# Performance work log

Measured on AMD Instinct MI355X. Metric: run time of the kernel, lower is better.

The kernel has to match this reference:

```python
import jax, jax.numpy as jnp
import numpy as np

V = 50257   # vocab_size
BLOCK = 1024
D = 768     # n_embd
H = 12      # n_head
L = 2       # n_layer
B = 4
T = 1024
EPS = 1e-5


def _ln(x, g, b):
    mu = jnp.mean(x, axis=-1, keepdims=True)
    var = jnp.var(x, axis=-1, keepdims=True)
    return (x - mu) * jax.lax.rsqrt(var + EPS) * g + b


def setup_inputs() -> dict:
    key = jax.random.key(0)
    ks = jax.random.split(key, 10)
    def n(k, shape, std=0.02):
        return jax.random.normal(k, shape, jnp.float32) * std
    proj_std = (2 * L) ** -0.5  # set_scale init in the torch code
    return dict(
        idx=jax.random.randint(ks[0], (B, T), 0, V),
        layer_num=0,
        wte=n(ks[1], (V, D)),
        wpe=n(ks[2], (BLOCK, D)),
        ln1_g=jnp.ones((L, D)), ln1_b=jnp.zeros((L, D)),
        attn_w=n(ks[3], (L, D, 3 * D)), attn_b=jnp.zeros((L, 3 * D)),
        proj_w=n(ks[4], (L, D, D), proj_std), proj_b=jnp.zeros((L, D)),
        ln2_g=jnp.ones((L, D)), ln2_b=jnp.zeros((L, D)),
        fc_w=n(ks[5], (L, D, 4 * D)), fc_b=jnp.zeros((L, 4 * D)),
        fc2_w=n(ks[6], (L, 4 * D, D), proj_std), fc2_b=jnp.zeros((L, D)),
        lnf_g=jnp.ones((D,)), lnf_b=jnp.zeros((D,)),
        lm_w=n(ks[7], (D, V)),
    )


def _gpt(idx, wte, wpe, ln1_g, ln1_b, attn_w, attn_b, proj_w, proj_b,
         ln2_g, ln2_b, fc_w, fc_b, fc2_w, fc2_b, lnf_g, lnf_b, lm_w):
    b, t = idx.shape
    hd = D // H
    x = wte[idx] + wpe[:t]                      # [B,T,D]
    causal = jnp.tril(jnp.ones((t, t), bool))   # [T,T]
    for l in range(L):
        h = _ln(x, ln1_g[l], ln1_b[l])
        qkv = h @ attn_w[l] + attn_b[l]          # [B,T,3D]
        q, k, v = jnp.split(qkv, 3, axis=-1)
        q = q.reshape(b, t, H, hd)
        k = k.reshape(b, t, H, hd)
        v = v.reshape(b, t, H, hd)
        att = jnp.einsum('bqhd,bkhd->bhqk', q, k) * (1.0 / np.sqrt(hd))
        att = jnp.where(causal, att, -jnp.inf)
        att = jax.nn.softmax(att, axis=-1)
        y = jnp.einsum('bhqk,bkhd->bqhd', att, v).reshape(b, t, D)
        x = x + (y @ proj_w[l] + proj_b[l])
        h2 = _ln(x, ln2_g[l], ln2_b[l])
        h2 = jax.nn.gelu(h2 @ fc_w[l] + fc_b[l], approximate=True)  # tanh GELU
        x = x + (h2 @ fc2_w[l] + fc2_b[l])
    x = _ln(x, lnf_g, lnf_b)
    return x @ lm_w                             # [B,T,V] logits


def reference(idx, layer_num, wte, wpe, ln1_g, ln1_b, attn_w, attn_b,
              proj_w, proj_b, ln2_g, ln2_b, fc_w, fc_b, fc2_w, fc2_b,
              lnf_g, lnf_b, lm_w):
    # layer_num is unused in the forward math (pipeline-stage bookkeeping)
    return _gpt(idx, wte, wpe, ln1_g, ln1_b, attn_w, attn_b, proj_w, proj_b,
                ln2_g, ln2_b, fc_w, fc_b, fc2_w, fc2_b, lnf_g, lnf_b, lm_w)
```

## Files before the change

kernel.cpp:

```cpp
#include <hip/hip_runtime.h>
#include <hip/hip_bf16.h>
#include <cstdint>
#include <cstddef>

typedef __bf16 bf16_t;
typedef __bf16 bf16x8 __attribute__((ext_vector_type(8)));
typedef float f32x4 __attribute__((ext_vector_type(4)));

#define GLB_AS(p) ((__attribute__((address_space(1))) void*)(void*)(p))
#define LDS_AS(p) ((__attribute__((address_space(3))) void*)(p))
#define PIN(x) asm volatile("" : "+v"(x))

__device__ __forceinline__ float wave_red_sum(float v) {
#pragma unroll
  for (int o = 1; o < 64; o <<= 1) v += __shfl_xor(v, o, 64);
  return v;
}

__device__ __forceinline__ float gelu_tanh(float v) {
  float c = 0.7978845608028654f * (v + 0.044715f * v * v * v);
  return 0.5f * v * (1.0f + tanhf(c));
}

__device__ __forceinline__ f32x4 mfma16(f32x4 a, f32x4 b, f32x4 c) {
  return __builtin_amdgcn_mfma_f32_16x16x32_bf16(
      __builtin_bit_cast(bf16x8, a), __builtin_bit_cast(bf16x8, b), c, 0, 0, 0);
}

__device__ __forceinline__ int swz(int off) { return off ^ ((off >> 3) & 0x70); }

__global__ __launch_bounds__(256) void embed_k(const int* __restrict__ idx,
                                               const float* __restrict__ wte,
                                               const float* __restrict__ wpe,
                                               float* __restrict__ x) {
  const int m = blockIdx.x;
  const int tid = threadIdx.x;
  const int tok = idx[m];
  const int t = m & 1023;
#pragma unroll
  for (int i = 0; i < 3; ++i) {
    const int d = tid + i * 256;
    x[(size_t)m * 768 + d] = wte[(size_t)tok * 768 + d] + wpe[(size_t)t * 768 + d];
  }
}

__global__ __launch_bounds__(256) void ln_k(const float* __restrict__ x,
                                            const float* __restrict__ g,
                                            const float* __restrict__ b,
                                            bf16_t* __restrict__ out) {
  const int row = blockIdx.x;
  const int tid = threadIdx.x;
  const float* xr = x + (size_t)row * 768;
  float v0 = xr[tid], v1 = xr[tid + 256], v2 = xr[tid + 512];
  float s = v0 + v1 + v2;
  float q = v0 * v0 + v1 * v1 + v2 * v2;
  s = wave_red_sum(s);
  q = wave_red_sum(q);
  __shared__ float sm[8];
  const int wave = tid >> 6, lane = tid & 63;
  if (lane == 0) { sm[wave] = s; sm[4 + wave] = q; }
  __syncthreads();
  s = sm[0] + sm[1] + sm[2] + sm[3];
  q = sm[4] + sm[5] + sm[6] + sm[7];
  const float mu = s * (1.0f / 768.0f);
  const float var = q * (1.0f / 768.0f) - mu * mu;
  const float rs = rsqrtf(var + 1e-5f);
  bf16_t* orow = out + (size_t)row * 768;
#pragma unroll
  for (int i = 0; i < 3; ++i) {
    const int d = tid + i * 256;
    const float v = (i == 0 ? v0 : (i == 1 ? v1 : v2));
    orow[d] = (bf16_t)((v - mu) * rs * g[d] + b[d]);
  }
}

__global__ __launch_bounds__(256) void transp_k(const float* __restrict__ W,
                                                bf16_t* __restrict__ WT,
                                                int K, int N, int Npad) {
  __shared__ float tile[32][33];
  const int n0 = blockIdx.x * 32, k0 = blockIdx.y * 32;
  const int tx = threadIdx.x, ty = threadIdx.y;
#pragma unroll
  for (int i = 0; i < 4; ++i) {
    const int k = k0 + ty + i * 8, n = n0 + tx;
    tile[ty + i * 8][tx] = (k < K && n < N) ? W[(size_t)k * N + n] : 0.0f;
  }
  __syncthreads();
#pragma unroll
  for (int i = 0; i < 4; ++i) {
    const int n = n0 + ty + i * 8, k = k0 + tx;
    if (n < Npad && k < K) WT[(size_t)n * K + k] = (bf16_t)tile[tx][ty + i * 8];
  }
}

__global__ __launch_bounds__(256) void vtr_k(const bf16_t* __restrict__ qkv,
                                             bf16_t* __restrict__ vt) {
  __shared__ bf16_t tile[64][72];
  const int bh = blockIdx.y;
  const int h = bh % 12, b = bh / 12;
  const int t0 = blockIdx.x * 64;
  const int tx = threadIdx.x & 63;
  const int wv = threadIdx.x >> 6;
#pragma unroll
  for (int i = 0; i < 16; ++i) {
    const int r = wv * 16 + i;
    tile[r][tx] = qkv[(size_t)(b * 1024 + t0 + r) * 2304 + 1536 + h * 64 + tx];
  }
  __syncthreads();
#pragma unroll
  for (int i = 0; i < 16; ++i) {
    const int d = wv * 16 + i;
    vt[((size_t)bh * 64 + d) * 1024 + t0 + tx] = tile[tx][d];
  }
}

template <int EPI>
__global__ __launch_bounds__(512, 2) void gemm256(const bf16_t* __restrict__ A,
                                                  const bf16_t* __restrict__ BT,
                                                  const float* __restrict__ bias,
                                                  void* __restrict__ outp,
                                                  int M, int N, int K, int Nout) {
  __shared__ __align__(16) char lds[131072];
  const int tid = threadIdx.x;
  const int lane = tid & 63, wave = tid >> 6;
  const int wr = wave >> 2, wc = wave & 3;
  const int fr = lane & 15, fq = lane >> 4;

  const int nmblk = M >> 8;
  const int nwg = gridDim.x;
  const int flat = blockIdx.x;
  const int xcd = flat & 7, rest = flat >> 3;
  const int q8 = nwg >> 3, r8 = nwg & 7;
  const int wgid = (xcd < r8 ? xcd * (q8 + 1) : r8 * (q8 + 1) + (xcd - r8) * q8) + rest;
  const int m0 = (wgid % nmblk) << 8;
  const int n0 = (wgid / nmblk) << 8;

  const int NT = K >> 6;

  int srow[4], scb[4];
#pragma unroll
  for (int u = 0; u < 4; ++u) {
    const int s = swz(u * 8192 + tid * 16);
    srow[u] = s >> 7;
    scb[u] = s & 127;
  }
  const char* Abase = (const char*)A;
  const char* Bbase = (const char*)BT;

  auto stageA = [&](int pi, int u, int tau) {
    const char* src = Abase + ((size_t)(m0 + srow[u]) * K + tau * 64) * 2 + scb[u];
    __builtin_amdgcn_global_load_lds(GLB_AS(src),
        LDS_AS(&lds[pi * 32768 + u * 8192 + wave * 1024]), 16, 0, 0);
  };
  auto stageB = [&](int pi, int u, int tau) {
    const char* src = Bbase + ((size_t)(n0 + srow[u]) * K + tau * 64) * 2 + scb[u];
    __builtin_amdgcn_global_load_lds(GLB_AS(src),
        LDS_AS(&lds[65536 + pi * 32768 + u * 8192 + wave * 1024]), 16, 0, 0);
  };
  auto rdA = [&](int pi, int msub, int i, int kk) -> f32x4 {
    const int row = wr * 128 + msub * 64 + i * 16 + fr;
    const int off = swz(row * 128 + kk * 64 + fq * 16);
    return *(const f32x4*)(&lds[pi * 32768 + off]);
  };
  auto rdB = [&](int pi, int j, int kk) -> f32x4 {
    const int row = wc * 64 + j * 16 + fr;
    const int off = swz(row * 128 + kk * 64 + fq * 16);
    return *(const f32x4*)(&lds[65536 + pi * 32768 + off]);
  };

  f32x4 acc[8][4] = {};
  f32x4 a_[4][2], b_[4][2];

  stageA(0, 0, 0); stageA(0, 1, 0); stageA(0, 2, 0); stageA(0, 3, 0);
  stageB(0, 0, 0); stageB(0, 1, 0); stageB(0, 2, 0); stageB(0, 3, 0);
  stageA(1, 0, 1); stageA(1, 2, 1); stageB(1, 0, 1); stageB(1, 1, 1);
  stageA(1, 1, 1); stageA(1, 3, 1);
  asm volatile("s_waitcnt vmcnt(6)" ::: "memory");
  __builtin_amdgcn_s_barrier();

  int pi = 0;
  for (int tau = 0; tau < NT; ++tau) {
#pragma unroll
    for (int i = 0; i < 4; ++i) { a_[i][0] = rdA(pi, 0, i, 0); a_[i][1] = rdA(pi, 0, i, 1); }
#pragma unroll
    for (int j = 0; j < 4; ++j) { b_[j][0] = rdB(pi, j, 0); b_[j][1] = rdB(pi, j, 1); }
#pragma unroll
    for (int i = 0; i < 4; ++i) { PIN(a_[i][0]); PIN(a_[i][1]); }
#pragma unroll
    for (int j = 0; j < 4; ++j) { PIN(b_[j][0]); PIN(b_[j][1]); }
    if (tau + 1 < NT) { stageB(pi ^ 1, 2, tau + 1); stageB(pi ^ 1, 3, tau + 1); }
    __builtin_amdgcn_s_barrier();
    __builtin_amdgcn_s_setprio(1);
#pragma unroll
    for (int i = 0; i < 4; ++i)
#pragma unroll
      for (int j = 0; j < 2; ++j) {
        acc[i][j] = mfma16(a_[i][0], b_[j][0], acc[i][j]);
        acc[i][j] = mfma16(a_[i][1], b_[j][1], acc[i][j]);
      }
    __builtin_amdgcn_s_setprio(0);
    __builtin_amdgcn_s_barrier();
    if (tau + 2 < NT) { stageA(pi, 0, tau + 2); stageA(pi, 2, tau + 2); }
    __builtin_amdgcn_s_barrier();
    __builtin_amdgcn_s_setprio(1);
#pragma unroll
    for (int i = 0; i < 4; ++i)
#pragma unroll
      for (int j = 0; j < 2; ++j) {
        acc[i][2 + j] = mfma16(a_[i][0], b_[2 + j][0], acc[i][2 + j]);
        acc[i][2 + j] = mfma16(a_[i][1], b_[2 + j][1], acc[i][2 + j]);
      }
    __builtin_amdgcn_s_setprio(0);
    __builtin_amdgcn_s_barrier();
#pragma unroll
    for (int i = 0; i < 4; ++i) { a_[i][0] = rdA(pi, 1, i, 0); a_[i][1] = rdA(pi, 1, i, 1); }
#pragma unroll
    for (int i = 0; i < 4; ++i) { PIN(a_[i][0]); PIN(a_[i][1]); }
    if (tau + 2 < NT) { stageB(pi, 0, tau + 2); stageB(pi, 1, tau + 2); }
    __builtin_amdgcn_s_barrier();
    __builtin_amdgcn_s_setprio(1);
#pragma unroll
    for (int i = 0; i < 4; ++i)
#pragma unroll
      for (int j = 0; j < 2; ++j) {
        acc[4 + i][j] = mfma16(a_[i][0], b_[j][0], acc[4 + i][j]);
        acc[4 + i][j] = mfma16(a_[i][1], b_[j][1], acc[4 + i][j]);
      }
    __builtin_amdgcn_s_setprio(0);
    __builtin_amdgcn_s_barrier();
    if (tau + 2 < NT) {
      stageA(pi, 1, tau + 2); stageA(pi, 3, tau + 2);
      asm volatile("s_waitcnt vmcnt(6)" ::: "memory");
    } else {
      asm volatile("s_waitcnt vmcnt(0)" ::: "memory");
    }
    __builtin_amdgcn_s_barrier();
    __builtin_amdgcn_s_setprio(1);
#pragma unroll
    for (int i = 0; i < 4; ++i)
#pragma unroll
      for (int j = 0; j < 2; ++j) {
        acc[4 + i][2 + j] = mfma16(a_[i][0], b_[2 + j][0], acc[4 + i][2 + j]);
        acc[4 + i][2 + j] = mfma16(a_[i][1], b_[2 + j][1], acc[4 + i][2 + j]);
      }
    __builtin_amdgcn_s_setprio(0);
    __builtin_amdgcn_s_barrier();
    pi ^= 1;
  }

#pragma unroll
  for (int i8 = 0; i8 < 8; ++i8) {
#pragma unroll
    for (int j4 = 0; j4 < 4; ++j4) {
      const int r0 = m0 + wr * 128 + i8 * 16 + fq * 4;
      const int c = n0 + wc * 64 + j4 * 16 + fr;
      float bv = 0.0f;
      if constexpr (EPI != 3) bv = bias[c];
#pragma unroll
      for (int e = 0; e < 4; ++e) {
        const int r = r0 + e;
        float v = acc[i8][j4][e] + bv;
        if constexpr (EPI == 0) {
          ((bf16_t*)outp)[(size_t)r * N + c] = (bf16_t)v;
        } else if constexpr (EPI == 1) {
          ((bf16_t*)outp)[(size_t)r * N + c] = (bf16_t)gelu_tanh(v);
        } else {
          if (c < Nout) ((float*)outp)[(size_t)r * Nout + c] = v;
        }
      }
    }
  }
}

template <int EPI>
__global__ __launch_bounds__(256) void gemm_bt(const bf16_t* __restrict__ A,
                                               const bf16_t* __restrict__ BT,
                                               const float* __restrict__ bias,
                                               void* __restrict__ outp,
                                               float* __restrict__ resid,
                                               int M, int N, int K, int Nout) {
  __shared__ __align__(16) bf16_t As[128 * 32];
  __shared__ __align__(16) bf16_t Bs[128 * 32];
  const int tid = threadIdx.x;
  const int lane = tid & 63, wave = tid >> 6;

  const int nmblk = M >> 7;
  const int nwg = gridDim.x;
  const int flat = blockIdx.x;
  const int xcd = flat & 7, rest = flat >> 3;
  const int q8 = nwg >> 3, r8 = nwg & 7;
  const int wgid = (xcd < r8 ? xcd * (q8 + 1) : r8 * (q8 + 1) + (xcd - r8) * q8) + rest;
  const int m0 = (wgid % nmblk) * 128;
  const int n0 = (wgid / nmblk) * 128;

  const int wr = wave >> 1, wc = wave & 1;
  const int fr = lane & 15, fq = lane >> 4;
  const int se = tid * 8;
  const int srow = se >> 5, scol = se & 31;
  const int wvbase = wave * 512;
  f32x4 acc[4][4] = {};

  for (int k0 = 0; k0 < K; k0 += 32) {
#pragma unroll
    for (int r = 0; r < 2; ++r) {
      __builtin_amdgcn_global_load_lds(
          GLB_AS(&A[(size_t)(m0 + srow + r * 64) * K + k0 + scol]),
          LDS_AS(&As[wvbase + r * 2048]), 16, 0, 0);
      __builtin_amdgcn_global_load_lds(
          GLB_AS(&BT[(size_t)(n0 + srow + r * 64) * K + k0 + scol]),
          LDS_AS(&Bs[wvbase + r * 2048]), 16, 0, 0);
    }
    __syncthreads();
    bf16x8 a[4], b[4];
#pragma unroll
    for (int i = 0; i < 4; ++i) {
      a[i] = *(const bf16x8*)(&As[(wr * 64 + i * 16 + fr) * 32 + fq * 8]);
      b[i] = *(const bf16x8*)(&Bs[(wc * 64 + i * 16 + fr) * 32 + fq * 8]);
    }
#pragma unroll
    for (int i = 0; i < 4; ++i)
#pragma unroll
      for (int j = 0; j < 4; ++j)
        acc[i][j] = __builtin_amdgcn_mfma_f32_16x16x32_bf16(a[i], b[j], acc[i][j], 0, 0, 0);
    __syncthreads();
  }

#pragma unroll
  for (int i = 0; i < 4; ++i) {
#pragma unroll
    for (int j = 0; j < 4; ++j) {
      const int r0 = m0 + wr * 64 + i * 16 + fq * 4;
      const int c = n0 + wc * 64 + j * 16 + fr;
      const float bv = bias[c];
#pragma unroll
      for (int e = 0; e < 4; ++e) {
        const int r = r0 + e;
        resid[(size_t)r * N + c] += acc[i][j][e] + bv;
      }
    }
  }
}

__global__ __launch_bounds__(256) void fattn_k(const bf16_t* __restrict__ qkv,
                                               const bf16_t* __restrict__ vt,
                                               bf16_t* __restrict__ y) {
  __shared__ bf16_t Pl[4][16][40];
  const int wave = threadIdx.x >> 6, lane = threadIdx.x & 63;
  const int wid = blockIdx.x * 4 + wave;
  const int qt = wid & 63;
  const int bh = wid >> 6;
  const int h = bh % 12, b = bh / 12;
  const int fr = lane & 15, fq = lane >> 4;

  const bf16_t* qrow = qkv + (size_t)(b * 1024 + qt * 16 + fr) * 2304 + h * 64;
  const bf16x8 qf0 = *(const bf16x8*)(qrow + fq * 8);
  const bf16x8 qf1 = *(const bf16x8*)(qrow + 32 + fq * 8);

  const bf16_t* kbase = qkv + (size_t)b * 1024 * 2304 + 768 + h * 64 + fq * 8;
  const bf16_t* vbase = vt + ((size_t)bh * 64 + fr) * 1024 + fq * 8;

  f32x4 o[4] = {};
  float mrun[4], lrun[4];
#pragma unroll
  for (int e = 0; e < 4; ++e) { mrun[e] = -1e30f; lrun[e] = 0.0f; }

  const int qg = qt * 16 + fq * 4;
  const int kv_end = qt * 16 + 16;

  for (int kv0 = 0; kv0 < kv_end; kv0 += 32) {
    f32x4 s0 = {}, s1 = {};
    {
      const bf16_t* k0p = kbase + (size_t)(kv0 + fr) * 2304;
      const bf16_t* k1p = kbase + (size_t)(kv0 + 16 + fr) * 2304;
      const bf16x8 kf00 = *(const bf16x8*)(k0p);
      const bf16x8 kf01 = *(const bf16x8*)(k0p + 32);
      const bf16x8 kf10 = *(const bf16x8*)(k1p);
      const bf16x8 kf11 = *(const bf16x8*)(k1p + 32);
      s0 = __builtin_amdgcn_mfma_f32_16x16x32_bf16(qf0, kf00, s0, 0, 0, 0);
      s0 = __builtin_amdgcn_mfma_f32_16x16x32_bf16(qf1, kf01, s0, 0, 0, 0);
      s1 = __builtin_amdgcn_mfma_f32_16x16x32_bf16(qf0, kf10, s1, 0, 0, 0);
      s1 = __builtin_amdgcn_mfma_f32_16x16x32_bf16(qf1, kf11, s1, 0, 0, 0);
    }
    float v0[4], v1[4];
#pragma unroll
    for (int e = 0; e < 4; ++e) {
      v0[e] = (kv0 + fr <= qg + e) ? s0[e] * 0.125f : -1e30f;
      v1[e] = (kv0 + 16 + fr <= qg + e) ? s1[e] * 0.125f : -1e30f;
    }
    float p0[4], p1[4];
#pragma unroll
    for (int e = 0; e < 4; ++e) {
      float mx = fmaxf(v0[e], v1[e]);
      mx = fmaxf(mx, __shfl_xor(mx, 1, 64));
      mx = fmaxf(mx, __shfl_xor(mx, 2, 64));
      mx = fmaxf(mx, __shfl_xor(mx, 4, 64));
      mx = fmaxf(mx, __shfl_xor(mx, 8, 64));
      const float mnew = fmaxf(mrun[e], mx);
      p0[e] = __expf(v0[e] - mnew);
      p1[e] = __expf(v1[e] - mnew);
      float rs = p0[e] + p1[e];
      rs += __shfl_xor(rs, 1, 64);
      rs += __shfl_xor(rs, 2, 64);
      rs += __shfl_xor(rs, 4, 64);
      rs += __shfl_xor(rs, 8, 64);
      const float alpha = __expf(mrun[e] - mnew);
      lrun[e] = lrun[e] * alpha + rs;
      mrun[e] = mnew;
#pragma unroll
      for (int db = 0; db < 4; ++db) o[db][e] *= alpha;
    }
#pragma unroll
    for (int e = 0; e < 4; ++e) {
      Pl[wave][fq * 4 + e][fr] = (bf16_t)p0[e];
      Pl[wave][fq * 4 + e][16 + fr] = (bf16_t)p1[e];
    }
    asm volatile("s_waitcnt lgkmcnt(0)" ::: "memory");
    const bf16x8 pf = *(const bf16x8*)(&Pl[wave][fr][fq * 8]);
#pragma unroll
    for (int db = 0; db < 4; ++db) {
      const bf16x8 vf = *(const bf16x8*)(vbase + (size_t)db * 16 * 1024 + kv0);
      o[db] = __builtin_amdgcn_mfma_f32_16x16x32_bf16(pf, vf, o[db], 0, 0, 0);
    }
  }

#pragma unroll
  for (int db = 0; db < 4; ++db) {
#pragma unroll
    for (int e = 0; e < 4; ++e) {
      const int q = qt * 16 + fq * 4 + e;
      const int d = db * 16 + fr;
      y[(size_t)(b * 1024 + q) * 768 + h * 64 + d] = (bf16_t)(o[db][e] / lrun[e]);
    }
  }
}

extern "C" void kernel_launch(void* const* d_in, const int* in_sizes, int n_in,
                              void* d_out, int out_size, void* d_ws, size_t ws_size,
                              hipStream_t stream) {
  constexpr int Bb = 4, T = 1024, Lg = 2, Vr = 50257, Vp = 50432;
  constexpr int M = Bb * T;

  const int* idx = (const int*)d_in[0];
  const float* wte = (const float*)d_in[2];
  const float* wpe = (const float*)d_in[3];
  const float* ln1_g = (const float*)d_in[4];
  const float* ln1_b = (const float*)d_in[5];
  const float* attn_w = (const float*)d_in[6];
  const float* attn_b = (const float*)d_in[7];
  const float* proj_w = (const float*)d_in[8];
  const float* proj_b = (const float*)d_in[9];
  const float* ln2_g = (const float*)d_in[10];
  const float* ln2_b = (const float*)d_in[11];
  const float* fc_w = (const float*)d_in[12];
  const float* fc_b = (const float*)d_in[13];
  const float* fc2_w = (const float*)d_in[14];
  const float* fc2_b = (const float*)d_in[15];
  const float* lnf_g = (const float*)d_in[16];
  const float* lnf_b = (const float*)d_in[17];
  const float* lm_w = (const float*)d_in[18];
  float* out = (float*)d_out;

  char* wp = (char*)d_ws;
  auto take = [&](size_t n) { char* p = wp; wp += (n + 255) & ~(size_t)255; return p; };
  bf16_t* WqkvT = (bf16_t*)take((size_t)Lg * 2304 * 768 * 2);
  bf16_t* WprojT = (bf16_t*)take((size_t)Lg * 768 * 768 * 2);
  bf16_t* WfcT = (bf16_t*)take((size_t)Lg * 3072 * 768 * 2);
  bf16_t* Wfc2T = (bf16_t*)take((size_t)Lg * 768 * 3072 * 2);
  bf16_t* WlmT = (bf16_t*)take((size_t)Vp * 768 * 2);
  float* xb = (float*)take((size_t)M * 768 * 4);
  bf16_t* hb = (bf16_t*)take((size_t)M * 768 * 2);
  bf16_t* qkvb = (bf16_t*)take((size_t)M * 2304 * 2);
  bf16_t* yb = (bf16_t*)take((size_t)M * 768 * 2);
  bf16_t* actb = (bf16_t*)take((size_t)M * 3072 * 2);
  bf16_t* vtb = (bf16_t*)take((size_t)M * 768 * 2);

  const dim3 tb(32, 8);
  for (int l = 0; l < Lg; ++l) {
    transp_k<<<dim3(2304 / 32, 768 / 32), tb, 0, stream>>>(
        attn_w + (size_t)l * 768 * 2304, WqkvT + (size_t)l * 2304 * 768, 768, 2304, 2304);
    transp_k<<<dim3(768 / 32, 768 / 32), tb, 0, stream>>>(
        proj_w + (size_t)l * 768 * 768, WprojT + (size_t)l * 768 * 768, 768, 768, 768);
    transp_k<<<dim3(3072 / 32, 768 / 32), tb, 0, stream>>>(
        fc_w + (size_t)l * 768 * 3072, WfcT + (size_t)l * 3072 * 768, 768, 3072, 3072);
    transp_k<<<dim3(768 / 32, 3072 / 32), tb, 0, stream>>>(
        fc2_w + (size_t)l * 3072 * 768, Wfc2T + (size_t)l * 768 * 3072, 3072, 768, 768);
  }
  transp_k<<<dim3(Vp / 32, 768 / 32), tb, 0, stream>>>(lm_w, WlmT, 768, Vr, Vp);

  embed_k<<<M, 256, 0, stream>>>(idx, wte, wpe, xb);

  for (int l = 0; l < Lg; ++l) {
    ln_k<<<M, 256, 0, stream>>>(xb, ln1_g + l * 768, ln1_b + l * 768, hb);
    gemm256<0><<<(M / 256) * (2304 / 256), 512, 0, stream>>>(
        hb, WqkvT + (size_t)l * 2304 * 768, attn_b + l * 2304, qkvb, M, 2304, 768, 2304);
    vtr_k<<<dim3(T / 64, Bb * 12), 256, 0, stream>>>(qkvb, vtb);
    fattn_k<<<(Bb * 12 * 64) / 4, 256, 0, stream>>>(qkvb, vtb, yb);
    gemm_bt<2><<<(M / 128) * (768 / 128), 256, 0, stream>>>(
        yb, WprojT + (size_t)l * 768 * 768, proj_b + l * 768, nullptr, xb,
        M, 768, 768, 768);
    ln_k<<<M, 256, 0, stream>>>(xb, ln2_g + l * 768, ln2_b + l * 768, hb);
    gemm256<1><<<(M / 256) * (3072 / 256), 512, 0, stream>>>(
        hb, WfcT + (size_t)l * 3072 * 768, fc_b + l * 3072, actb, M, 3072, 768, 3072);
    gemm_bt<2><<<(M / 128) * (768 / 128), 256, 0, stream>>>(
        actb, Wfc2T + (size_t)l * 768 * 3072, fc2_b + l * 768, nullptr, xb,
        M, 768, 3072, 768);
  }
  ln_k<<<M, 256, 0, stream>>>(xb, lnf_g, lnf_b, hb);
  gemm256<3><<<(M / 256) * (Vp / 256), 512, 0, stream>>>(
      hb, WlmT, nullptr, out, M, Vp, 768, Vr);
}
```

Before: 1.249 ms.

## Make 256-tile GEMM persistent with cross-tile prefetch pipelining

Converts the 256x256 GEMM into a persistent kernel where each workgroup processes a contiguous range of output tiles. The global-to-LDS prefetch keeps running across tile boundaries, so the loads for the next tile overlap the current tile's tail and epilogue. The LM head now launches a fixed grid of 512 workgroups instead of one per tile, which cuts launch waves and tail effects. The QKV and FC GEMMs keep one tile per block. The cost is extra index bookkeeping per k-step and a serialized epilogue inside each workgroup.

```diff
diff --git a/kernel.cpp b/kernel.cpp
--- a/kernel.cpp
+++ b/kernel.cpp
@@ -115,11 +115,12 @@
 }
 
 template <int EPI>
-__global__ __launch_bounds__(512, 2) void gemm256(const bf16_t* __restrict__ A,
-                                                  const bf16_t* __restrict__ BT,
-                                                  const float* __restrict__ bias,
-                                                  void* __restrict__ outp,
-                                                  int M, int N, int K, int Nout) {
+__global__ __launch_bounds__(512, 2) void gemm256p(const bf16_t* __restrict__ A,
+                                                   const bf16_t* __restrict__ BT,
+                                                   const float* __restrict__ bias,
+                                                   void* __restrict__ outp,
+                                                   int M, int N, int K, int Nout,
+                                                   int ntiles) {
   __shared__ __align__(16) char lds[131072];
   const int tid = threadIdx.x;
   const int lane = tid & 63, wave = tid >> 6;
@@ -127,15 +128,17 @@
   const int fr = lane & 15, fq = lane >> 4;
 
   const int nmblk = M >> 8;
-  const int nwg = gridDim.x;
+  const int G = gridDim.x;
   const int flat = blockIdx.x;
   const int xcd = flat & 7, rest = flat >> 3;
-  const int q8 = nwg >> 3, r8 = nwg & 7;
-  const int wgid = (xcd < r8 ? xcd * (q8 + 1) : r8 * (q8 + 1) + (xcd - r8) * q8) + rest;
-  const int m0 = (wgid % nmblk) << 8;
-  const int n0 = (wgid / nmblk) << 8;
-
+  const int q8 = G >> 3, r8 = G & 7;
+  const int bid = (xcd < r8 ? xcd * (q8 + 1) : r8 * (q8 + 1) + (xcd - r8) * q8) + rest;
+  const int qt = ntiles / G, rt = ntiles % G;
+  const int tstart = bid * qt + (bid < rt ? bid : rt);
+  const int cnt = qt + (bid < rt ? 1 : 0);
+  if (cnt == 0) return;
   const int NT = K >> 6;
+  const int sEnd = (tstart + cnt) * NT;
 
   int srow[4], scb[4];
 #pragma unroll
@@ -147,13 +150,13 @@
   const char* Abase = (const char*)A;
   const char* Bbase = (const char*)BT;
 
-  auto stageA = [&](int pi, int u, int tau) {
-    const char* src = Abase + ((size_t)(m0 + srow[u]) * K + tau * 64) * 2 + scb[u];
+  auto stageA = [&](int pi, int u, int m0x, int tauK) {
+    const char* src = Abase + ((size_t)(m0x + srow[u]) * K + tauK * 64) * 2 + scb[u];
     __builtin_amdgcn_global_load_lds(GLB_AS(src),
         LDS_AS(&lds[pi * 32768 + u * 8192 + wave * 1024]), 16, 0, 0);
   };
-  auto stageB = [&](int pi, int u, int tau) {
-    const char* src = Bbase + ((size_t)(n0 + srow[u]) * K + tau * 64) * 2 + scb[u];
+  auto stageB = [&](int pi, int u, int n0x, int tauK) {
+    const char* src = Bbase + ((size_t)(n0x + srow[u]) * K + tauK * 64) * 2 + scb[u];
     __builtin_amdgcn_global_load_lds(GLB_AS(src),
         LDS_AS(&lds[65536 + pi * 32768 + u * 8192 + wave * 1024]), 16, 0, 0);
   };
@@ -168,107 +171,125 @@
     return *(const f32x4*)(&lds[65536 + pi * 32768 + off]);
   };
 
+  int m0 = (tstart % nmblk) << 8, n0 = (tstart / nmblk) << 8;
+  int m1 = m0, n1 = n0, t1 = 1;
+  int m2 = m0, n2 = n0, t2 = 2;
+  auto adv = [&](int& mx, int& nx, int& tx) {
+    if (++tx == NT) { tx = 0; mx += 256; if (mx >= M) { mx = 0; nx += 256; } }
+  };
+
   f32x4 acc[8][4] = {};
   f32x4 a_[4][2], b_[4][2];
 
-  stageA(0, 0, 0); stageA(0, 1, 0); stageA(0, 2, 0); stageA(0, 3, 0);
-  stageB(0, 0, 0); stageB(0, 1, 0); stageB(0, 2, 0); stageB(0, 3, 0);
-  stageA(1, 0, 1); stageA(1, 2, 1); stageB(1, 0, 1); stageB(1, 1, 1);
-  stageA(1, 1, 1); stageA(1, 3, 1);
+  stageA(0, 0, m0, 0); stageA(0, 1, m0, 0); stageA(0, 2, m0, 0); stageA(0, 3, m0, 0);
+  stageB(0, 0, n0, 0); stageB(0, 1, n0, 0); stageB(0, 2, n0, 0); stageB(0, 3, n0, 0);
+  stageA(1, 0, m1, t1); stageA(1, 2, m1, t1); stageB(1, 0, n1, t1); stageB(1, 1, n1, t1);
+  stageA(1, 1, m1, t1); stageA(1, 3, m1, t1);
   asm volatile("s_waitcnt vmcnt(6)" ::: "memory");
   __builtin_amdgcn_s_barrier();
 
   int pi = 0;
-  for (int tau = 0; tau < NT; ++tau) {
-#pragma unroll
-    for (int i = 0; i < 4; ++i) { a_[i][0] = rdA(pi, 0, i, 0); a_[i][1] = rdA(pi, 0, i, 1); }
-#pragma unroll
-    for (int j = 0; j < 4; ++j) { b_[j][0] = rdB(pi, j, 0); b_[j][1] = rdB(pi, j, 1); }
-#pragma unroll
-    for (int i = 0; i < 4; ++i) { PIN(a_[i][0]); PIN(a_[i][1]); }
-#pragma unroll
-    for (int j = 0; j < 4; ++j) { PIN(b_[j][0]); PIN(b_[j][1]); }
-    if (tau + 1 < NT) { stageB(pi ^ 1, 2, tau + 1); stageB(pi ^ 1, 3, tau + 1); }
-    __builtin_amdgcn_s_barrier();
-    __builtin_amdgcn_s_setprio(1);
-#pragma unroll
-    for (int i = 0; i < 4; ++i)
-#pragma unroll
-      for (int j = 0; j < 2; ++j) {
-        acc[i][j] = mfma16(a_[i][0], b_[j][0], acc[i][j]);
-        acc[i][j] = mfma16(a_[i][1], b_[j][1], acc[i][j]);
+  int s = tstart * NT;
+  for (int t = 0; t < cnt; ++t) {
+    for (int tau = 0; tau < NT; ++tau, ++s) {
+      const bool h1 = (s + 1 < sEnd), h2 = (s + 2 < sEnd);
+#pragma unroll
+      for (int i = 0; i < 4; ++i) { a_[i][0] = rdA(pi, 0, i, 0); a_[i][1] = rdA(pi, 0, i, 1); }
+#pragma unroll
+      for (int j = 0; j < 4; ++j) { b_[j][0] = rdB(pi, j, 0); b_[j][1] = rdB(pi, j, 1); }
+#pragma unroll
+      for (int i = 0; i < 4; ++i) { PIN(a_[i][0]); PIN(a_[i][1]); }
+#pragma unroll
+      for (int j = 0; j < 4; ++j) { PIN(b_[j][0]); PIN(b_[j][1]); }
+      if (h1) { stageB(pi ^ 1, 2, n1, t1); stageB(pi ^ 1, 3, n1, t1); }
+      __builtin_amdgcn_s_barrier();
+      __builtin_amdgcn_s_setprio(1);
+#pragma unroll
+      for (int i = 0; i < 4; ++i)
+#pragma unroll
+        for (int j = 0; j < 2; ++j) {
+          acc[i][j] = mfma16(a_[i][0], b_[j][0], acc[i][j]);
+          acc[i][j] = mfma16(a_[i][1], b_[j][1], acc[i][j]);
+        }
+      __builtin_amdgcn_s_setprio(0);
+      __builtin_amdgcn_s_barrier();
+      if (h2) { stageA(pi, 0, m2, t2); stageA(pi, 2, m2, t2); }
+      __builtin_amdgcn_s_barrier();
+      __builtin_amdgcn_s_setprio(1);
+#pragma unroll
+      for (int i = 0; i < 4; ++i)
+#pragma unroll
+        for (int j = 0; j < 2; ++j) {
+          acc[i][2 + j] = mfma16(a_[i][0], b_[2 + j][0], acc[i][2 + j]);
+          acc[i][2 + j] = mfma16(a_[i][1], b_[2 + j][1], acc[i][2 + j]);
+        }
+      __builtin_amdgcn_s_setprio(0);
+      __builtin_amdgcn_s_barrier();
+#pragma unroll
+      for (int i = 0; i < 4; ++i) { a_[i][0] = rdA(pi, 1, i, 0); a_[i][1] = rdA(pi, 1, i, 1); }
+#pragma unroll
+      for (int i = 0; i < 4; ++i) { PIN(a_[i][0]); PIN(a_[i][1]); }
+      if (h2) { stageB(pi, 0, n2, t2); stageB(pi, 1, n2, t2); }
+      __builtin_amdgcn_s_barrier();
+      __builtin_amdgcn_s_setprio(1);
+#pragma unroll
+      for (int i = 0; i < 4; ++i)
+#pragma unroll
+        for (int j = 0; j < 2; ++j) {
+          acc[4 + i][j] = mfma16(a_[i][0], b_[j][0], acc[4 + i][j]);
+          acc[4 + i][j] = mfma16(a_[i][1], b_[j][1], acc[4 + i][j]);
+        }
+      __builtin_amdgcn_s_setprio(0);
+      __builtin_amdgcn_s_barrier();
+      if (h2) {
+        stageA(pi, 1, m2, t2); stageA(pi, 3, m2, t2);
+        asm volatile("s_waitcnt vmcnt(6)" ::: "memory");
+      } else {
+        asm volatile("s_waitcnt vmcnt(0)" ::: "memory");
       }
-    __builtin_amdgcn_s_setprio(0);
-    __builtin_amdgcn_s_barrier();
-    if (tau + 2 < NT) { stageA(pi, 0, tau + 2); stageA(pi, 2, tau + 2); }
-    __builtin_amdgcn_s_barrier();
-    __builtin_amdgcn_s_setprio(1);
-#pragma unroll
-    for (int i = 0; i < 4; ++i)
-#pragma unroll
-      for (int j = 0; j < 2; ++j) {
-        acc[i][2 + j] = mfma16(a_[i][0], b_[2 + j][0], acc[i][2 + j]);
-        acc[i][2 + j] = mfma16(a_[i][1], b_[2 + j][1], acc[i][2 + j]);
-      }
-    __builtin_amdgcn_s_setprio(0);
-    __builtin_amdgcn_s_barrier();
-#pragma unroll
-    for (int i = 0; i < 4; ++i) { a_[i][0] = rdA(pi, 1, i, 0); a_[i][1] = rdA(pi, 1, i, 1); }
-#pragma unroll
-    for (int i = 0; i < 4; ++i) { PIN(a_[i][0]); PIN(a_[i][1]); }
-    if (tau + 2 < NT) { stageB(pi, 0, tau + 2); stageB(pi, 1, tau + 2); }
-    __builtin_amdgcn_s_barrier();
-    __builtin_amdgcn_s_setprio(1);
-#pragma unroll
-    for (int i = 0; i < 4; ++i)
-#pragma unroll
-      for (int j = 0; j < 2; ++j) {
-        acc[4 + i][j] = mfma16(a_[i][0], b_[j][0], acc[4 + i][j]);
-        acc[4 + i][j] = mfma16(a_[i][1], b_[j][1], acc[4 + i][j]);
-      }
-    __builtin_amdgcn_s_setprio(0);
-    __builtin_amdgcn_s_barrier();
-    if (tau + 2 < NT) {
-      stageA(pi, 1, tau + 2); stageA(pi, 3, tau + 2);
-      asm volatile("s_waitcnt vmcnt(6)" ::: "memory");
-    } else {
-      asm volatile("s_waitcnt vmcnt(0)" ::: "memory");
-    }
-    __builtin_amdgcn_s_barrier();
-    __builtin_amdgcn_s_setprio(1);
-#pragma unroll
-    for (int i = 0; i < 4; ++i)
-#pragma unroll
-      for (int j = 0; j < 2; ++j) {
-        acc[4 + i][2 + j] = mfma16(a_[i][0], b_[2 + j][0], acc[4 + i][2 + j]);
-        acc[4 + i][2 + j] = mfma16(a_[i][1], b_[2 + j][1], acc[4 + i][2 + j]);
-      }
-    __builtin_amdgcn_s_setprio(0);
-    __builtin_amdgcn_s_barrier();
-    pi ^= 1;
-  }
-
-#pragma unroll
-  for (int i8 = 0; i8 < 8; ++i8) {
-#pragma unroll
-    for (int j4 = 0; j4 < 4; ++j4) {
-      const int r0 = m0 + wr * 128 + i8 * 16 + fq * 4;
-      const int c = n0 + wc * 64 + j4 * 16 + fr;
-      float bv = 0.0f;
-      if constexpr (EPI != 3) bv = bias[c];
-#pragma unroll
-      for (int e = 0; e < 4; ++e) {
-        const int r = r0 + e;
-        float v = acc[i8][j4][e] + bv;
-        if constexpr (EPI == 0) {
-          ((bf16_t*)outp)[(size_t)r * N + c] = (bf16_t)v;
-        } else if constexpr (EPI == 1) {
-          ((bf16_t*)outp)[(size_t)r * N + c] = (bf16_t)gelu_tanh(v);
-        } else {
-          if (c < Nout) ((float*)outp)[(size_t)r * Nout + c] = v;
+      __builtin_amdgcn_s_barrier();
+      __builtin_amdgcn_s_setprio(1);
+#pragma unroll
+      for (int i = 0; i < 4; ++i)
+#pragma unroll
+        for (int j = 0; j < 2; ++j) {
+          acc[4 + i][2 + j] = mfma16(a_[i][0], b_[2 + j][0], acc[4 + i][2 + j]);
+          acc[4 + i][2 + j] = mfma16(a_[i][1], b_[2 + j][1], acc[4 + i][2 + j]);
+        }
+      __builtin_amdgcn_s_setprio(0);
+      __builtin_amdgcn_s_barrier();
+      pi ^= 1;
+      adv(m1, n1, t1);
+      adv(m2, n2, t2);
+    }
+
+#pragma unroll
+    for (int i8 = 0; i8 < 8; ++i8) {
+#pragma unroll
+      for (int j4 = 0; j4 < 4; ++j4) {
+        const int r0 = m0 + wr * 128 + i8 * 16 + fq * 4;
+        const int c = n0 + wc * 64 + j4 * 16 + fr;
+        float bv = 0.0f;
+        if constexpr (EPI != 3) bv = bias[c];
+#pragma unroll
+        for (int e = 0; e < 4; ++e) {
+          const int r = r0 + e;
+          float v = acc[i8][j4][e] + bv;
+          if constexpr (EPI == 0) {
+            ((bf16_t*)outp)[(size_t)r * N + c] = (bf16_t)v;
+          } else if constexpr (EPI == 1) {
+            ((bf16_t*)outp)[(size_t)r * N + c] = (bf16_t)gelu_tanh(v);
+          } else {
+            if (c < Nout) ((float*)outp)[(size_t)r * Nout + c] = v;
+          }
         }
       }
     }
+#pragma unroll
+    for (int i8 = 0; i8 < 8; ++i8)
+#pragma unroll
+      for (int j4 = 0; j4 < 4; ++j4) acc[i8][j4] = (f32x4){0.0f, 0.0f, 0.0f, 0.0f};
+    m0 += 256; if (m0 >= M) { m0 = 0; n0 += 256; }
   }
 }
 
@@ -491,21 +512,23 @@
 
   for (int l = 0; l < Lg; ++l) {
     ln_k<<<M, 256, 0, stream>>>(xb, ln1_g + l * 768, ln1_b + l * 768, hb);
-    gemm256<0><<<(M / 256) * (2304 / 256), 512, 0, stream>>>(
-        hb, WqkvT + (size_t)l * 2304 * 768, attn_b + l * 2304, qkvb, M, 2304, 768, 2304);
+    gemm256p<0><<<(M / 256) * (2304 / 256), 512, 0, stream>>>(
+        hb, WqkvT + (size_t)l * 2304 * 768, attn_b + l * 2304, qkvb,
+        M, 2304, 768, 2304, (M / 256) * (2304 / 256));
     vtr_k<<<dim3(T / 64, Bb * 12), 256, 0, stream>>>(qkvb, vtb);
     fattn_k<<<(Bb * 12 * 64) / 4, 256, 0, stream>>>(qkvb, vtb, yb);
     gemm_bt<2><<<(M / 128) * (768 / 128), 256, 0, stream>>>(
         yb, WprojT + (size_t)l * 768 * 768, proj_b + l * 768, nullptr, xb,
         M, 768, 768, 768);
     ln_k<<<M, 256, 0, stream>>>(xb, ln2_g + l * 768, ln2_b + l * 768, hb);
-    gemm256<1><<<(M / 256) * (3072 / 256), 512, 0, stream>>>(
-        hb, WfcT + (size_t)l * 3072 * 768, fc_b + l * 3072, actb, M, 3072, 768, 3072);
+    gemm256p<1><<<(M / 256) * (3072 / 256), 512, 0, stream>>>(
+        hb, WfcT + (size_t)l * 3072 * 768, fc_b + l * 3072, actb,
+        M, 3072, 768, 3072, (M / 256) * (3072 / 256));
     gemm_bt<2><<<(M / 128) * (768 / 128), 256, 0, stream>>>(
         actb, Wfc2T + (size_t)l * 768 * 3072, fc2_b + l * 768, nullptr, xb,
         M, 768, 3072, 768);
   }
   ln_k<<<M, 256, 0, stream>>>(xb, lnf_g, lnf_b, hb);
-  gemm256<3><<<(M / 256) * (Vp / 256), 512, 0, stream>>>(
-      hb, WlmT, nullptr, out, M, Vp, 768, Vr);
-}
+  gemm256p<3><<<512, 512, 0, stream>>>(
+      hb, WlmT, nullptr, out, M, Vp, 768, Vr, (M / 256) * (Vp / 256));
+}
```

New measurement: 1.251 ms. Within noise of the previous version (+0.1%).
